# Optimization experiments

Measured on AMD Instinct MI355X. Metric: run time of the kernel, lower is better.

The kernel has to match this reference:

```python
import jax, jax.numpy as jnp
import numpy as np
from jax import lax

B, T, I, H = 64, 512, 1024, 1024


def setup_inputs() -> dict:
    key = jax.random.key(0)
    ks = jax.random.split(key, 10)
    stdv = 1.0 / np.sqrt(H)
    u = lambda k, shp: jax.random.uniform(k, shp, jnp.float32, -stdv, stdv)
    return {
        "x": jax.random.normal(ks[0], (B, T, I), jnp.float32),
        "hx": jax.random.normal(ks[1], (B, H), jnp.float32),
        "cx": jax.random.normal(ks[2], (B, H), jnp.float32),
        "weight_ih": u(ks[3], (4 * H, I)),
        "weight_hh": u(ks[4], (4 * H, H)),
        "bias_ih": u(ks[5], (4 * H,)),
        "bias_hh": u(ks[6], (4 * H,)),
        "weight_ch_i": u(ks[7], (H,)),
        "weight_ch_f": u(ks[8], (H,)),
        "weight_ch_o": u(ks[9], (H,)),
    }


def reference(x, hx, cx, weight_ih, weight_hh, bias_ih, bias_hh,
              weight_ch_i, weight_ch_f, weight_ch_o):
    # Peephole LSTM over time. Note: original module returns the INITIAL
    # (hx, cx) as the state output (faithful to source).
    bias = bias_ih + bias_hh  # fuse the two bias adds

    def step(carry, x_t):
        h, c = carry  # [B,H] each
        xh = x_t @ weight_ih.T + h @ weight_hh.T + bias  # [B,4H]
        i, f, g, o = jnp.split(xh, 4, axis=1)
        i = jax.nn.sigmoid(i + weight_ch_i * c)
        f = jax.nn.sigmoid(f + weight_ch_f * c)
        g = jnp.tanh(g)
        cy = f * c + i * g
        o = jax.nn.sigmoid(o + weight_ch_o * cy)
        hy = o * jnp.tanh(cy)
        return (hy, cy), hy

    xs = jnp.swapaxes(x, 0, 1)  # [T,B,I]
    _, hs = lax.scan(step, (hx, cx), xs)  # hs: [T,B,H]
    hidden_seq = jnp.swapaxes(hs, 0, 1)  # [B,T,H]
    return hidden_seq, (hx, cx)
```

## Files before the change

### kernel.cpp

```cpp
#include <hip/hip_runtime.h>
#include <hip/hip_bf16.h>
#include <cstdint>
#include <cstddef>

#define BB 64
#define TT 512
#define II 1024
#define HH 1024
#define NSLOT 256

typedef __attribute__((ext_vector_type(8))) short bf16x8;
typedef __attribute__((ext_vector_type(4))) float f32x4;
typedef __attribute__((ext_vector_type(8))) ushort ushort8v;
typedef __attribute__((ext_vector_type(2))) unsigned long long u64x2;

#define OFF_WHH   0ull
#define OFF_WIH   8388608ull
#define OFF_BIAS  16777216ull
#define OFF_CNT   16793600ull
#define OFF_HROT  16801792ull
#define OFF_HBUF  83910656ull
#define OFF_CBUF  84172800ull
#define OFF_PRE   84434944ull
#define OFF_XB_B  84434944ull
#define NEED_A    352870400ull
#define NEED_B    151543808ull

__device__ __forceinline__ ushort f2b(float f) {
  union { float f; uint32_t u; } v; v.f = f;
  uint32_t r = v.u + 0x7fffu + ((v.u >> 16) & 1u);
  return (ushort)(r >> 16);
}
__device__ __forceinline__ float b2f(ushort u) {
  union { uint32_t u; float f; } v; v.u = ((uint32_t)u) << 16; return v.f;
}
__device__ __forceinline__ float sigm(float x) { return 1.0f / (1.0f + __expf(-x)); }
__device__ __forceinline__ float tanh_f(float x) {
  float e = __expf(2.0f * x);
  return 1.0f - 2.0f / (e + 1.0f);
}

__global__ void k_prep(const float* __restrict__ wih, const float* __restrict__ whh,
                       const float* __restrict__ bih, const float* __restrict__ bhh,
                       const float* __restrict__ hx, const float* __restrict__ cx,
                       ushort* __restrict__ Whh_b, ushort* __restrict__ Wih_b,
                       float* __restrict__ bias, ushort* __restrict__ hbuf0,
                       float* __restrict__ cbuf, uint32_t* __restrict__ hrot,
                       int* __restrict__ cnt) {
  const int tid = blockIdx.x * blockDim.x + threadIdx.x;
  const int nth = gridDim.x * blockDim.x;
  for (int idx = tid; idx < 4096 * 128; idx += nth) {
    const size_t o = (size_t)idx * 8;
    f32x4 h0 = *(const f32x4*)(whh + o), h1 = *(const f32x4*)(whh + o + 4);
    f32x4 i0 = *(const f32x4*)(wih + o), i1 = *(const f32x4*)(wih + o + 4);
    ushort8v a, b;
    a[0]=f2b(h0[0]); a[1]=f2b(h0[1]); a[2]=f2b(h0[2]); a[3]=f2b(h0[3]);
    a[4]=f2b(h1[0]); a[5]=f2b(h1[1]); a[6]=f2b(h1[2]); a[7]=f2b(h1[3]);
    b[0]=f2b(i0[0]); b[1]=f2b(i0[1]); b[2]=f2b(i0[2]); b[3]=f2b(i0[3]);
    b[4]=f2b(i1[0]); b[5]=f2b(i1[1]); b[6]=f2b(i1[2]); b[7]=f2b(i1[3]);
    *(ushort8v*)(Whh_b + o) = a;
    *(ushort8v*)(Wih_b + o) = b;
  }
  for (int idx = tid; idx < 4096; idx += nth) bias[idx] = bih[idx] + bhh[idx];
  for (int idx = tid; idx < BB * HH; idx += nth) {
    const ushort hb = f2b(hx[idx]);
    hbuf0[idx] = hb;
    cbuf[idx] = cx[idx];
    hrot[idx] = (uint32_t)hb;
  }
  for (int idx = tid; idx < 512 * 4; idx += nth) cnt[idx] = 0;
}

__global__ void k_convx_tb(const float* __restrict__ x, ushort* __restrict__ xb) {
  const int tid = blockIdx.x * blockDim.x + threadIdx.x;
  const int nth = gridDim.x * blockDim.x;
  for (int idx = tid; idx < TT * BB * (II / 8); idx += nth) {
    const int i8 = idx & 127;
    const int tb = idx >> 7;
    const int t = tb >> 6, b = tb & 63;
    const float* src = x + ((size_t)b * TT + t) * II + (size_t)i8 * 8;
    f32x4 v0 = *(const f32x4*)src, v1 = *(const f32x4*)(src + 4);
    ushort8v o;
    o[0]=f2b(v0[0]); o[1]=f2b(v0[1]); o[2]=f2b(v0[2]); o[3]=f2b(v0[3]);
    o[4]=f2b(v1[0]); o[5]=f2b(v1[1]); o[6]=f2b(v1[2]); o[7]=f2b(v1[3]);
    *(ushort8v*)(xb + (size_t)idx * 8) = o;
  }
}

template<bool FASTA>
__global__ void __launch_bounds__(256)
k_gemm(const ushort* __restrict__ xb, const float* __restrict__ xf,
       const ushort* __restrict__ Wih, ushort* __restrict__ pre) {
  __shared__ ushort As[2][8192];
  __shared__ ushort Bs[2][8192];
  const int tid = threadIdx.x;
  const int lane = tid & 63;
  const int w = tid >> 6;
  const int wm = w & 1, wn = w >> 1;
  const int l15 = lane & 15, kg = lane >> 4;
  const int work = (blockIdx.x & 7) * 1024 + (blockIdx.x >> 3);
  const int rp = work >> 5, cp = work & 31;
  const int m0 = rp * 128, n0 = cp * 128;

  f32x4 acc[4][4];
#pragma unroll
  for (int i = 0; i < 4; ++i)
#pragma unroll
    for (int j = 0; j < 4; ++j) acc[i][j] = f32x4{0.f, 0.f, 0.f, 0.f};

  bf16x8 ra[4], rb[4];

#define LOADTILE(KT)                                                          \
  {                                                                           \
    _Pragma("unroll")                                                         \
    for (int it = 0; it < 4; ++it) {                                          \
      const int idx = it * 256 + tid;                                         \
      const int row = idx >> 3, seg = idx & 7;                                \
      if (FASTA) {                                                            \
        ra[it] = *(const bf16x8*)(xb + (size_t)(m0 + row) * 1024 + (KT) * 64 + seg * 8); \
      } else {                                                                \
        const float* s = xf + (size_t)(m0 + row) * 1024 + (KT) * 64 + seg * 8;\
        f32x4 v0 = *(const f32x4*)s, v1 = *(const f32x4*)(s + 4);             \
        bf16x8 o;                                                             \
        o[0]=(short)f2b(v0[0]); o[1]=(short)f2b(v0[1]);                       \
        o[2]=(short)f2b(v0[2]); o[3]=(short)f2b(v0[3]);                       \
        o[4]=(short)f2b(v1[0]); o[5]=(short)f2b(v1[1]);                       \
        o[6]=(short)f2b(v1[2]); o[7]=(short)f2b(v1[3]);                       \
        ra[it] = o;                                                           \
      }                                                                       \
      rb[it] = *(const bf16x8*)(Wih + (size_t)(n0 + row) * 1024 + (KT) * 64 + seg * 8); \
    }                                                                         \
  }

#define WRITETILE(BUF)                                                        \
  {                                                                           \
    _Pragma("unroll")                                                         \
    for (int it = 0; it < 4; ++it) {                                          \
      const int idx = it * 256 + tid;                                         \
      const int row = idx >> 3, seg = idx & 7;                                \
      const int off = row * 64 + ((seg ^ (row & 7)) << 3);                    \
      *(bf16x8*)(&As[BUF][off]) = ra[it];                                     \
      *(bf16x8*)(&Bs[BUF][off]) = rb[it];                                     \
    }                                                                         \
  }

  LOADTILE(0);
  WRITETILE(0);
  __syncthreads();

#pragma unroll 1
  for (int kt = 0; kt < 16; ++kt) {
    const int cur = kt & 1;
    if (kt < 15) LOADTILE(kt + 1);
#pragma unroll
    for (int ks = 0; ks < 2; ++ks) {
      bf16x8 af[4], bf_[4];
      const int koff = ks * 32 + kg * 8;
      const int swz = koff ^ ((l15 & 7) << 3);
#pragma unroll
      for (int i = 0; i < 4; ++i) {
        const int arow = wm * 64 + i * 16 + l15;
        af[i] = *(const bf16x8*)(&As[cur][arow * 64 + swz]);
        const int brow = wn * 64 + i * 16 + l15;
        bf_[i] = *(const bf16x8*)(&Bs[cur][brow * 64 + swz]);
      }
#pragma unroll
      for (int i = 0; i < 4; ++i)
#pragma unroll
        for (int j = 0; j < 4; ++j)
          acc[i][j] = __builtin_amdgcn_mfma_f32_16x16x32_bf16(af[i], bf_[j], acc[i][j], 0, 0, 0);
    }
    if (kt < 15) WRITETILE(cur ^ 1);
    __syncthreads();
  }

#pragma unroll
  for (int i = 0; i < 4; ++i)
#pragma unroll
    for (int j = 0; j < 4; ++j)
#pragma unroll
      for (int e = 0; e < 4; ++e) {
        const int m = m0 + wm * 64 + i * 16 + kg * 4 + e;
        const int n = n0 + wn * 64 + j * 16 + l15;
        pre[((size_t)(m & 511) * 64 + (m >> 9)) * 4096 + n] = f2b(acc[i][j][e]);
      }
#undef LOADTILE
#undef WRITETILE
}

__global__ void __launch_bounds__(256, 1)
k_recur(const ushort* __restrict__ Whh_b, const float* __restrict__ bias,
        uint32_t* __restrict__ hrot, const ushort* __restrict__ pre,
        const float* __restrict__ cx,
        const float* __restrict__ wci, const float* __restrict__ wcf,
        const float* __restrict__ wco, float* __restrict__ out,
        int* __restrict__ cnt) {
  __shared__ float red[4][4][16][17];
  const int tid = threadIdx.x;
  const int lane = tid & 63;
  const int w = tid >> 6;
  const int l15 = lane & 15, kg = lane >> 4;
  const int g = blockIdx.x & 3, j = blockIdx.x >> 2;

  bf16x8 wf[4][8];
#pragma unroll
  for (int gate = 0; gate < 4; ++gate)
#pragma unroll
    for (int ks = 0; ks < 8; ++ks)
      wf[gate][ks] = *(const bf16x8*)(Whh_b
          + (size_t)(gate * 1024 + j * 16 + l15) * 1024 + (w * 8 + ks) * 32 + kg * 8);

  const int grow = tid >> 4, ghl = tid & 15;
  const int brow = g * 16 + grow;
  const int hidx = j * 16 + ghl;
  const float bi = bias[hidx], bff = bias[1024 + hidx],
              bg = bias[2048 + hidx], bo = bias[3072 + hidx];
  const float pci = wci[hidx], pcf = wcf[hidx], pco = wco[hidx];
  float creg = cx[brow * 1024 + hidx];

  const int rowoff = (g * 16 + l15) * 1024 + w * 256 + kg * 8;

  const ushort* pp0 = pre + ((size_t)brow) * 4096 + hidx;
  float pxi = b2f(pp0[0]), pxf = b2f(pp0[1024]),
        pxg = b2f(pp0[2048]), pxo = b2f(pp0[3072]);

#pragma unroll 1
  for (int t = 0; t < 512; ++t) {
    const int tn = (t < 511) ? (t + 1) : 511;
    const ushort* pp = pre + ((size_t)tn * 64 + brow) * 4096 + hidx;
    const ushort ru0 = pp[0], ru1 = pp[1024], ru2 = pp[2048], ru3 = pp[3072];

    if (t > 0) {
      const int* cp = &cnt[t * 4 + g];
      while (__hip_atomic_load(cp, __ATOMIC_RELAXED, __HIP_MEMORY_SCOPE_AGENT) < 64)
        __builtin_amdgcn_s_sleep(1);
    }

    const unsigned long long* hq =
        (const unsigned long long*)(hrot + (size_t)(t & (NSLOT - 1)) * 65536 + rowoff);
    const unsigned long long pat =
        ((unsigned long long)(uint32_t)t << 48) | ((unsigned long long)(uint32_t)t << 16);
    const unsigned long long MSK = 0xFFFF0000FFFF0000ULL;
    unsigned long long q[32];
#pragma unroll
    for (int ks = 0; ks < 8; ++ks) {
      u64x2 v0 = *(const u64x2*)(hq + ks * 16);
      u64x2 v1 = *(const u64x2*)(hq + ks * 16 + 2);
      q[ks * 4 + 0] = v0[0]; q[ks * 4 + 1] = v0[1];
      q[ks * 4 + 2] = v1[0]; q[ks * 4 + 3] = v1[1];
    }
    unsigned long long bad = 0;
#pragma unroll
    for (int qq = 0; qq < 32; ++qq) bad |= (q[qq] ^ pat) & MSK;
    while (bad) {
#pragma unroll
      for (int qq = 0; qq < 32; ++qq)
        if ((q[qq] ^ pat) & MSK)
          q[qq] = __hip_atomic_load(hq + (qq >> 2) * 16 + (qq & 3),
                                    __ATOMIC_RELAXED, __HIP_MEMORY_SCOPE_AGENT);
      bad = 0;
#pragma unroll
      for (int qq = 0; qq < 32; ++qq) bad |= (q[qq] ^ pat) & MSK;
    }
    bf16x8 af[8];
#pragma unroll
    for (int ks = 0; ks < 8; ++ks) {
      const unsigned long long v0 = q[ks * 4 + 0], v1 = q[ks * 4 + 1],
                               v2 = q[ks * 4 + 2], v3 = q[ks * 4 + 3];
      bf16x8 a;
      a[0] = (short)(v0 & 0xFFFF); a[1] = (short)((v0 >> 32) & 0xFFFF);
      a[2] = (short)(v1 & 0xFFFF); a[3] = (short)((v1 >> 32) & 0xFFFF);
      a[4] = (short)(v2 & 0xFFFF); a[5] = (short)((v2 >> 32) & 0xFFFF);
      a[6] = (short)(v3 & 0xFFFF); a[7] = (short)((v3 >> 32) & 0xFFFF);
      af[ks] = a;
    }

    f32x4 acc[4];
#pragma unroll
    for (int gate = 0; gate < 4; ++gate) acc[gate] = f32x4{0.f, 0.f, 0.f, 0.f};
#pragma unroll
    for (int ks = 0; ks < 8; ++ks)
#pragma unroll
      for (int gate = 0; gate < 4; ++gate)
        acc[gate] = __builtin_amdgcn_mfma_f32_16x16x32_bf16(af[ks], wf[gate][ks], acc[gate], 0, 0, 0);

#pragma unroll
    for (int gate = 0; gate < 4; ++gate)
#pragma unroll
      for (int e = 0; e < 4; ++e)
        red[w][gate][kg * 4 + e][l15] = acc[gate][e];
    __syncthreads();

    float s0 = 0.f, s1 = 0.f, s2 = 0.f, s3 = 0.f;
#pragma unroll
    for (int ww = 0; ww < 4; ++ww) {
      s0 += red[ww][0][grow][ghl];
      s1 += red[ww][1][grow][ghl];
      s2 += red[ww][2][grow][ghl];
      s3 += red[ww][3][grow][ghl];
    }
    const float ig = sigm(s0 + bi + pxi + pci * creg);
    const float fg = sigm(s1 + bff + pxf + pcf * creg);
    const float gg = tanh_f(s2 + bg + pxg);
    const float cy = fg * creg + ig * gg;
    const float og = sigm(s3 + bo + pxo + pco * cy);
    const float hy = og * tanh_f(cy);
    creg = cy;
    if (t < 511) {
      const uint32_t word = (((uint32_t)(t + 1)) << 16) | (uint32_t)f2b(hy);
      __hip_atomic_store(&hrot[(size_t)((t + 1) & (NSLOT - 1)) * 65536 + brow * 1024 + hidx],
                         word, __ATOMIC_RELAXED, __HIP_MEMORY_SCOPE_AGENT);
      if (tid == 0)
        __hip_atomic_fetch_add(&cnt[(t + 1) * 4 + g], 1, __ATOMIC_RELAXED,
                               __HIP_MEMORY_SCOPE_AGENT);
    }
    __builtin_nontemporal_store(hy, &out[(size_t)brow * 524288 + (size_t)t * 1024 + hidx]);
    pxi = b2f(ru0); pxf = b2f(ru1); pxg = b2f(ru2); pxo = b2f(ru3);
    __syncthreads();
  }
}

template<bool XB>
__global__ void __launch_bounds__(256)
k_step2(const ushort* __restrict__ Whh, const ushort* __restrict__ Wih,
        const float* __restrict__ bias,
        const ushort* __restrict__ hprev, ushort* __restrict__ hnext,
        float* __restrict__ cbuf, const ushort* __restrict__ xb,
        const float* __restrict__ x,
        const float* __restrict__ wci, const float* __restrict__ wcf,
        const float* __restrict__ wco, float* __restrict__ out, int t) {
  __shared__ float pre[32][33];
  const int lane = threadIdx.x & 63;
  const int w = threadIdx.x >> 6;
  const int mt = w & 1, ct = w >> 1;
  const int mg = blockIdx.x & 1, cg = blockIdx.x >> 1;
  const int l15 = lane & 15, kg = lane >> 4;
  const int arow = mg * 32 + mt * 16 + l15;
  const int gate = ct * 2 + (l15 >> 3);
  const int hl = l15 & 7;
  const int gcol = gate * HH + cg * 8 + hl;

  const ushort* wr = Whh + (size_t)gcol * 1024 + kg * 8;
  const ushort* hr = hprev + (size_t)arow * HH + kg * 8;

  f32x4 acc0 = {0.f,0.f,0.f,0.f};
  f32x4 acc1 = {0.f,0.f,0.f,0.f};

#pragma unroll 8
  for (int ks = 0; ks < 32; ks += 2) {
    bf16x8 a0 = *(const bf16x8*)(hr + ks * 32);
    bf16x8 b0 = *(const bf16x8*)(wr + ks * 32);
    acc0 = __builtin_amdgcn_mfma_f32_16x16x32_bf16(a0, b0, acc0, 0, 0, 0);
    bf16x8 a1 = *(const bf16x8*)(hr + ks * 32 + 32);
    bf16x8 b1 = *(const bf16x8*)(wr + ks * 32 + 32);
    acc1 = __builtin_amdgcn_mfma_f32_16x16x32_bf16(a1, b1, acc1, 0, 0, 0);
  }
  const ushort* wrx = Wih + (size_t)gcol * 1024 + kg * 8;
  if (XB) {
    const ushort* xr = xb + ((size_t)t * BB + arow) * II + kg * 8;
#pragma unroll 8
    for (int ks = 0; ks < 32; ks += 2) {
      bf16x8 a0 = *(const bf16x8*)(xr + ks * 32);
      bf16x8 b0 = *(const bf16x8*)(wrx + ks * 32);
      acc0 = __builtin_amdgcn_mfma_f32_16x16x32_bf16(a0, b0, acc0, 0, 0, 0);
      bf16x8 a1 = *(const bf16x8*)(xr + ks * 32 + 32);
      bf16x8 b1 = *(const bf16x8*)(wrx + ks * 32 + 32);
      acc1 = __builtin_amdgcn_mfma_f32_16x16x32_bf16(a1, b1, acc1, 0, 0, 0);
    }
  } else {
    const float* xr = x + ((size_t)arow * TT + t) * II + kg * 8;
#pragma unroll 4
    for (int ks = 0; ks < 32; ++ks) {
      f32x4 v0 = *(const f32x4*)(xr + ks * 32);
      f32x4 v1 = *(const f32x4*)(xr + ks * 32 + 4);
      bf16x8 a;
      a[0]=(short)f2b(v0[0]); a[1]=(short)f2b(v0[1]);
      a[2]=(short)f2b(v0[2]); a[3]=(short)f2b(v0[3]);
      a[4]=(short)f2b(v1[0]); a[5]=(short)f2b(v1[1]);
      a[6]=(short)f2b(v1[2]); a[7]=(short)f2b(v1[3]);
      bf16x8 b0 = *(const bf16x8*)(wrx + ks * 32);
      acc0 = __builtin_amdgcn_mfma_f32_16x16x32_bf16(a, b0, acc0, 0, 0, 0);
    }
  }
  f32x4 acc = acc0 + acc1;

  const float bv = bias[gcol];
  const int lr0 = mt * 16 + kg * 4;
  const int lc2 = ct * 16 + l15;
#pragma unroll
  for (int jj = 0; jj < 4; ++jj) pre[lr0 + jj][lc2] = acc[jj] + bv;
  __syncthreads();

  const int tid = threadIdx.x;
  const int lr = tid >> 3;
  const int hl2 = tid & 7;
  const int b = mg * 32 + lr;
  const int hi = cg * 8 + hl2;
  const float ip = pre[lr][hl2];
  const float fp = pre[lr][8 + hl2];
  const float gp = pre[lr][16 + hl2];
  const float op = pre[lr][24 + hl2];
  const float c = cbuf[b * HH + hi];
  const float ig = sigm(ip + wci[hi] * c);
  const float fg = sigm(fp + wcf[hi] * c);
  const float gg = tanh_f(gp);
  const float cy = fg * c + ig * gg;
  const float og = sigm(op + wco[hi] * cy);
  const float hy = og * tanh_f(cy);
  cbuf[b * HH + hi] = cy;
  hnext[b * HH + hi] = f2b(hy);
  out[((size_t)b * TT + t) * HH + hi] = hy;
}

extern "C" void kernel_launch(void* const* d_in, const int* in_sizes, int n_in,
                              void* d_out, int out_size, void* d_ws, size_t ws_size,
                              hipStream_t stream) {
  const float* x   = (const float*)d_in[0];
  const float* hx  = (const float*)d_in[1];
  const float* cx  = (const float*)d_in[2];
  const float* wih = (const float*)d_in[3];
  const float* whh = (const float*)d_in[4];
  const float* bih = (const float*)d_in[5];
  const float* bhh = (const float*)d_in[6];
  const float* wci = (const float*)d_in[7];
  const float* wcf = (const float*)d_in[8];
  const float* wco = (const float*)d_in[9];
  float* out = (float*)d_out;

  char* ws = (char*)d_ws;
  ushort*   Whh_b = (ushort*)(ws + OFF_WHH);
  ushort*   Wih_b = (ushort*)(ws + OFF_WIH);
  float*    bias  = (float*)(ws + OFF_BIAS);
  int*      cnt   = (int*)(ws + OFF_CNT);
  uint32_t* hrot  = (uint32_t*)(ws + OFF_HROT);
  ushort*   hbuf  = (ushort*)(ws + OFF_HBUF);
  float*    cbuf  = (float*)(ws + OFF_CBUF);
  ushort*   pre   = (ushort*)(ws + OFF_PRE);

  k_prep<<<512, 256, 0, stream>>>(wih, whh, bih, bhh, hx, cx,
                                  Whh_b, Wih_b, bias, hbuf, cbuf, hrot, cnt);

  if (ws_size >= NEED_A) {
    k_gemm<false><<<8192, 256, 0, stream>>>(nullptr, x, Wih_b, pre);
    k_recur<<<256, 256, 0, stream>>>(Whh_b, bias, hrot, pre, cx,
                                     wci, wcf, wco, out, cnt);
  } else if (ws_size >= NEED_B) {
    ushort* xb = (ushort*)(ws + OFF_XB_B);
    k_convx_tb<<<1024, 256, 0, stream>>>(x, xb);
    for (int t = 0; t < TT; ++t) {
      const ushort* hp = hbuf + (size_t)(t & 1) * BB * HH;
      ushort* hn = hbuf + (size_t)((t + 1) & 1) * BB * HH;
      k_step2<true><<<256, 256, 0, stream>>>(Whh_b, Wih_b, bias, hp, hn, cbuf,
                                             xb, x, wci, wcf, wco, out, t);
    }
  } else {
    for (int t = 0; t < TT; ++t) {
      const ushort* hp = hbuf + (size_t)(t & 1) * BB * HH;
      ushort* hn = hbuf + (size_t)((t + 1) & 1) * BB * HH;
      k_step2<false><<<256, 256, 0, stream>>>(Whh_b, Wih_b, bias, hp, hn, cbuf,
                                              nullptr, x, wci, wcf, wco, out, t);
    }
  }

  hipMemcpyAsync(out + 33554432, hx, (size_t)BB * HH * 4,
                 hipMemcpyDeviceToDevice, stream);
  hipMemcpyAsync(out + 33554432 + 65536, cx, (size_t)BB * HH * 4,
                 hipMemcpyDeviceToDevice, stream);
}
```

Before: 2.889 ms.

## Drop counter barrier, shrink h ring to 4 slots, retile recurrence blocks

Removes the per-step atomic counter wait. Blocks now rely only on the timestamp tags embedded in each h word, with a short backoff sleep while polling. The h rotation buffer shrinks from 256 slots to 4, and prep marks the unused slots with an invalid tag. k_recur is retiled to 512 threads covering 8 batch rows by 32 hidden units, splitting K across 8 waves, which halves the h data each block polls. The risks are that a 4-slot ring allows overwrite races if blocks drift apart, and that the K-split doubles the shared-memory reduction, with half the threads idle during the gate math.

```diff
diff --git a/kernel.cpp b/kernel.cpp
--- a/kernel.cpp
+++ b/kernel.cpp
@@ -7,7 +7,7 @@
 #define TT 512
 #define II 1024
 #define HH 1024
-#define NSLOT 256
+#define NSLOT 4
 
 typedef __attribute__((ext_vector_type(8))) short bf16x8;
 typedef __attribute__((ext_vector_type(4))) float f32x4;
@@ -17,14 +17,13 @@
 #define OFF_WHH   0ull
 #define OFF_WIH   8388608ull
 #define OFF_BIAS  16777216ull
-#define OFF_CNT   16793600ull
-#define OFF_HROT  16801792ull
-#define OFF_HBUF  83910656ull
-#define OFF_CBUF  84172800ull
-#define OFF_PRE   84434944ull
-#define OFF_XB_B  84434944ull
-#define NEED_A    352870400ull
-#define NEED_B    151543808ull
+#define OFF_HROT  16793600ull
+#define OFF_HBUF  17842176ull
+#define OFF_CBUF  18104320ull
+#define OFF_PRE   18366464ull
+#define OFF_XB_B  18366464ull
+#define NEED_A    286801920ull
+#define NEED_B    85475328ull
 
 __device__ __forceinline__ ushort f2b(float f) {
   union { float f; uint32_t u; } v; v.f = f;
@@ -45,8 +44,7 @@
                        const float* __restrict__ hx, const float* __restrict__ cx,
                        ushort* __restrict__ Whh_b, ushort* __restrict__ Wih_b,
                        float* __restrict__ bias, ushort* __restrict__ hbuf0,
-                       float* __restrict__ cbuf, uint32_t* __restrict__ hrot,
-                       int* __restrict__ cnt) {
+                       float* __restrict__ cbuf, uint32_t* __restrict__ hrot) {
   const int tid = blockIdx.x * blockDim.x + threadIdx.x;
   const int nth = gridDim.x * blockDim.x;
   for (int idx = tid; idx < 4096 * 128; idx += nth) {
@@ -68,7 +66,8 @@
     cbuf[idx] = cx[idx];
     hrot[idx] = (uint32_t)hb;
   }
-  for (int idx = tid; idx < 512 * 4; idx += nth) cnt[idx] = 0;
+  for (int idx = tid; idx < 3 * 65536; idx += nth)
+    hrot[65536 + idx] = 0xFFFF0000u;
 }
 
 __global__ void k_convx_tb(const float* __restrict__ x, ushort* __restrict__ xb) {
@@ -188,134 +187,147 @@
 #undef WRITETILE
 }
 
-__global__ void __launch_bounds__(256, 1)
+__global__ void __launch_bounds__(512, 2)
 k_recur(const ushort* __restrict__ Whh_b, const float* __restrict__ bias,
         uint32_t* __restrict__ hrot, const ushort* __restrict__ pre,
         const float* __restrict__ cx,
         const float* __restrict__ wci, const float* __restrict__ wcf,
-        const float* __restrict__ wco, float* __restrict__ out,
-        int* __restrict__ cnt) {
-  __shared__ float red[4][4][16][17];
+        const float* __restrict__ wco, float* __restrict__ out) {
+  __shared__ float red[8][4][32][9];
   const int tid = threadIdx.x;
   const int lane = tid & 63;
   const int w = tid >> 6;
   const int l15 = lane & 15, kg = lane >> 4;
-  const int g = blockIdx.x & 3, j = blockIdx.x >> 2;
-
-  bf16x8 wf[4][8];
-#pragma unroll
-  for (int gate = 0; gate < 4; ++gate)
-#pragma unroll
-    for (int ks = 0; ks < 8; ++ks)
-      wf[gate][ks] = *(const bf16x8*)(Whh_b
-          + (size_t)(gate * 1024 + j * 16 + l15) * 1024 + (w * 8 + ks) * 32 + kg * 8);
-
-  const int grow = tid >> 4, ghl = tid & 15;
-  const int brow = g * 16 + grow;
-  const int hidx = j * 16 + ghl;
-  const float bi = bias[hidx], bff = bias[1024 + hidx],
-              bg = bias[2048 + hidx], bo = bias[3072 + hidx];
-  const float pci = wci[hidx], pcf = wcf[hidx], pco = wco[hidx];
-  float creg = cx[brow * 1024 + hidx];
-
-  const int rowoff = (g * 16 + l15) * 1024 + w * 256 + kg * 8;
-
-  const ushort* pp0 = pre + ((size_t)brow) * 4096 + hidx;
-  float pxi = b2f(pp0[0]), pxf = b2f(pp0[1024]),
-        pxg = b2f(pp0[2048]), pxo = b2f(pp0[3072]);
+  const int g = blockIdx.x & 7;
+  const int j = blockIdx.x >> 3;
+
+  bf16x8 wf[4][2][4];
+#pragma unroll
+  for (int gt = 0; gt < 4; ++gt)
+#pragma unroll
+    for (int ct = 0; ct < 2; ++ct)
+#pragma unroll
+      for (int ks = 0; ks < 4; ++ks)
+        wf[gt][ct][ks] = *(const bf16x8*)(Whh_b
+            + (size_t)(gt * 1024 + j * 32 + ct * 16 + l15) * 1024
+            + w * 128 + ks * 32 + kg * 8);
+
+  const int grow = tid & 7;
+  const int ghl = (tid >> 3) & 31;
+  const int brow = g * 8 + grow;
+  const int hidx = j * 32 + ghl;
+  float bi = 0, bff = 0, bg = 0, bo = 0, pci = 0, pcf = 0, pco = 0, creg = 0;
+  float pxi = 0, pxf = 0, pxg = 0, pxo = 0;
+  if (tid < 256) {
+    bi = bias[hidx]; bff = bias[1024 + hidx];
+    bg = bias[2048 + hidx]; bo = bias[3072 + hidx];
+    pci = wci[hidx]; pcf = wcf[hidx]; pco = wco[hidx];
+    creg = cx[brow * 1024 + hidx];
+    const ushort* pp0 = pre + ((size_t)brow) * 4096 + hidx;
+    pxi = b2f(pp0[0]); pxf = b2f(pp0[1024]);
+    pxg = b2f(pp0[2048]); pxo = b2f(pp0[3072]);
+  }
+
+  const int arow = g * 8 + (l15 & 7);
+  const unsigned long long MSK = 0xFFFF0000FFFF0000ULL;
 
 #pragma unroll 1
   for (int t = 0; t < 512; ++t) {
-    const int tn = (t < 511) ? (t + 1) : 511;
-    const ushort* pp = pre + ((size_t)tn * 64 + brow) * 4096 + hidx;
-    const ushort ru0 = pp[0], ru1 = pp[1024], ru2 = pp[2048], ru3 = pp[3072];
-
-    if (t > 0) {
-      const int* cp = &cnt[t * 4 + g];
-      while (__hip_atomic_load(cp, __ATOMIC_RELAXED, __HIP_MEMORY_SCOPE_AGENT) < 64)
-        __builtin_amdgcn_s_sleep(1);
-    }
-
-    const unsigned long long* hq =
-        (const unsigned long long*)(hrot + (size_t)(t & (NSLOT - 1)) * 65536 + rowoff);
+    ushort nx0 = 0, nx1 = 0, nx2 = 0, nx3 = 0;
+    if (tid < 256) {
+      const int tn = (t < 511) ? (t + 1) : 511;
+      const ushort* pp = pre + ((size_t)tn * 64 + brow) * 4096 + hidx;
+      nx0 = pp[0]; nx1 = pp[1024]; nx2 = pp[2048]; nx3 = pp[3072];
+    }
+
+    const unsigned long long* hq = (const unsigned long long*)
+        (hrot + (size_t)(t & (NSLOT - 1)) * 65536 + (size_t)arow * 1024
+         + w * 128 + kg * 8);
     const unsigned long long pat =
         ((unsigned long long)(uint32_t)t << 48) | ((unsigned long long)(uint32_t)t << 16);
-    const unsigned long long MSK = 0xFFFF0000FFFF0000ULL;
-    unsigned long long q[32];
-#pragma unroll
-    for (int ks = 0; ks < 8; ++ks) {
-      u64x2 v0 = *(const u64x2*)(hq + ks * 16);
-      u64x2 v1 = *(const u64x2*)(hq + ks * 16 + 2);
-      q[ks * 4 + 0] = v0[0]; q[ks * 4 + 1] = v0[1];
-      q[ks * 4 + 2] = v1[0]; q[ks * 4 + 3] = v1[1];
+    unsigned long long q[16];
+#pragma unroll
+    for (int ks = 0; ks < 4; ++ks) {
+      u64x2 a = *(const u64x2*)(hq + ks * 16);
+      u64x2 b = *(const u64x2*)(hq + ks * 16 + 2);
+      q[ks * 4 + 0] = a[0]; q[ks * 4 + 1] = a[1];
+      q[ks * 4 + 2] = b[0]; q[ks * 4 + 3] = b[1];
     }
     unsigned long long bad = 0;
 #pragma unroll
-    for (int qq = 0; qq < 32; ++qq) bad |= (q[qq] ^ pat) & MSK;
+    for (int qq = 0; qq < 16; ++qq) bad |= (q[qq] ^ pat) & MSK;
+    int spins = 0;
     while (bad) {
-#pragma unroll
-      for (int qq = 0; qq < 32; ++qq)
+      if (spins++ > 2) __builtin_amdgcn_s_sleep(1);
+#pragma unroll
+      for (int qq = 0; qq < 16; ++qq)
         if ((q[qq] ^ pat) & MSK)
           q[qq] = __hip_atomic_load(hq + (qq >> 2) * 16 + (qq & 3),
                                     __ATOMIC_RELAXED, __HIP_MEMORY_SCOPE_AGENT);
       bad = 0;
 #pragma unroll
-      for (int qq = 0; qq < 32; ++qq) bad |= (q[qq] ^ pat) & MSK;
-    }
-    bf16x8 af[8];
-#pragma unroll
-    for (int ks = 0; ks < 8; ++ks) {
+      for (int qq = 0; qq < 16; ++qq) bad |= (q[qq] ^ pat) & MSK;
+    }
+
+    f32x4 acc[4][2];
+#pragma unroll
+    for (int gt = 0; gt < 4; ++gt)
+#pragma unroll
+      for (int ct = 0; ct < 2; ++ct) acc[gt][ct] = f32x4{0.f, 0.f, 0.f, 0.f};
+#pragma unroll
+    for (int ks = 0; ks < 4; ++ks) {
       const unsigned long long v0 = q[ks * 4 + 0], v1 = q[ks * 4 + 1],
                                v2 = q[ks * 4 + 2], v3 = q[ks * 4 + 3];
-      bf16x8 a;
-      a[0] = (short)(v0 & 0xFFFF); a[1] = (short)((v0 >> 32) & 0xFFFF);
-      a[2] = (short)(v1 & 0xFFFF); a[3] = (short)((v1 >> 32) & 0xFFFF);
-      a[4] = (short)(v2 & 0xFFFF); a[5] = (short)((v2 >> 32) & 0xFFFF);
-      a[6] = (short)(v3 & 0xFFFF); a[7] = (short)((v3 >> 32) & 0xFFFF);
-      af[ks] = a;
-    }
-
-    f32x4 acc[4];
-#pragma unroll
-    for (int gate = 0; gate < 4; ++gate) acc[gate] = f32x4{0.f, 0.f, 0.f, 0.f};
-#pragma unroll
-    for (int ks = 0; ks < 8; ++ks)
-#pragma unroll
-      for (int gate = 0; gate < 4; ++gate)
-        acc[gate] = __builtin_amdgcn_mfma_f32_16x16x32_bf16(af[ks], wf[gate][ks], acc[gate], 0, 0, 0);
-
-#pragma unroll
-    for (int gate = 0; gate < 4; ++gate)
-#pragma unroll
-      for (int e = 0; e < 4; ++e)
-        red[w][gate][kg * 4 + e][l15] = acc[gate][e];
+      bf16x8 af;
+      af[0] = (short)(v0 & 0xFFFF); af[1] = (short)((v0 >> 32) & 0xFFFF);
+      af[2] = (short)(v1 & 0xFFFF); af[3] = (short)((v1 >> 32) & 0xFFFF);
+      af[4] = (short)(v2 & 0xFFFF); af[5] = (short)((v2 >> 32) & 0xFFFF);
+      af[6] = (short)(v3 & 0xFFFF); af[7] = (short)((v3 >> 32) & 0xFFFF);
+#pragma unroll
+      for (int gt = 0; gt < 4; ++gt)
+#pragma unroll
+        for (int ct = 0; ct < 2; ++ct)
+          acc[gt][ct] = __builtin_amdgcn_mfma_f32_16x16x32_bf16(
+              af, wf[gt][ct][ks], acc[gt][ct], 0, 0, 0);
+    }
+
+    if (kg < 2) {
+#pragma unroll
+      for (int gt = 0; gt < 4; ++gt)
+#pragma unroll
+        for (int ct = 0; ct < 2; ++ct)
+#pragma unroll
+          for (int e = 0; e < 4; ++e)
+            red[w][gt][ct * 16 + l15][kg * 4 + e] = acc[gt][ct][e];
+    }
     __syncthreads();
 
-    float s0 = 0.f, s1 = 0.f, s2 = 0.f, s3 = 0.f;
-#pragma unroll
-    for (int ww = 0; ww < 4; ++ww) {
-      s0 += red[ww][0][grow][ghl];
-      s1 += red[ww][1][grow][ghl];
-      s2 += red[ww][2][grow][ghl];
-      s3 += red[ww][3][grow][ghl];
-    }
-    const float ig = sigm(s0 + bi + pxi + pci * creg);
-    const float fg = sigm(s1 + bff + pxf + pcf * creg);
-    const float gg = tanh_f(s2 + bg + pxg);
-    const float cy = fg * creg + ig * gg;
-    const float og = sigm(s3 + bo + pxo + pco * cy);
-    const float hy = og * tanh_f(cy);
-    creg = cy;
-    if (t < 511) {
-      const uint32_t word = (((uint32_t)(t + 1)) << 16) | (uint32_t)f2b(hy);
-      __hip_atomic_store(&hrot[(size_t)((t + 1) & (NSLOT - 1)) * 65536 + brow * 1024 + hidx],
-                         word, __ATOMIC_RELAXED, __HIP_MEMORY_SCOPE_AGENT);
-      if (tid == 0)
-        __hip_atomic_fetch_add(&cnt[(t + 1) * 4 + g], 1, __ATOMIC_RELAXED,
-                               __HIP_MEMORY_SCOPE_AGENT);
-    }
-    __builtin_nontemporal_store(hy, &out[(size_t)brow * 524288 + (size_t)t * 1024 + hidx]);
-    pxi = b2f(ru0); pxf = b2f(ru1); pxg = b2f(ru2); pxo = b2f(ru3);
+    if (tid < 256) {
+      float s0 = 0.f, s1 = 0.f, s2 = 0.f, s3 = 0.f;
+#pragma unroll
+      for (int ww = 0; ww < 8; ++ww) {
+        s0 += red[ww][0][ghl][grow];
+        s1 += red[ww][1][ghl][grow];
+        s2 += red[ww][2][ghl][grow];
+        s3 += red[ww][3][ghl][grow];
+      }
+      const float ig = sigm(s0 + bi + pxi + pci * creg);
+      const float fg = sigm(s1 + bff + pxf + pcf * creg);
+      const float gg = tanh_f(s2 + bg + pxg);
+      const float cy = fg * creg + ig * gg;
+      const float og = sigm(s3 + bo + pxo + pco * cy);
+      const float hy = og * tanh_f(cy);
+      creg = cy;
+      if (t < 511) {
+        const uint32_t word = (((uint32_t)(t + 1)) << 16) | (uint32_t)f2b(hy);
+        __hip_atomic_store(&hrot[(size_t)((t + 1) & (NSLOT - 1)) * 65536
+                                 + brow * 1024 + hidx],
+                           word, __ATOMIC_RELAXED, __HIP_MEMORY_SCOPE_AGENT);
+      }
+      __builtin_nontemporal_store(hy,
+          &out[(size_t)brow * 524288 + (size_t)t * 1024 + hidx]);
+      pxi = b2f(nx0); pxf = b2f(nx1); pxg = b2f(nx2); pxo = b2f(nx3);
+    }
     __syncthreads();
   }
 }
@@ -431,19 +443,18 @@
   ushort*   Whh_b = (ushort*)(ws + OFF_WHH);
   ushort*   Wih_b = (ushort*)(ws + OFF_WIH);
   float*    bias  = (float*)(ws + OFF_BIAS);
-  int*      cnt   = (int*)(ws + OFF_CNT);
   uint32_t* hrot  = (uint32_t*)(ws + OFF_HROT);
   ushort*   hbuf  = (ushort*)(ws + OFF_HBUF);
   float*    cbuf  = (float*)(ws + OFF_CBUF);
   ushort*   pre   = (ushort*)(ws + OFF_PRE);
 
   k_prep<<<512, 256, 0, stream>>>(wih, whh, bih, bhh, hx, cx,
-                                  Whh_b, Wih_b, bias, hbuf, cbuf, hrot, cnt);
+                                  Whh_b, Wih_b, bias, hbuf, cbuf, hrot);
 
   if (ws_size >= NEED_A) {
     k_gemm<false><<<8192, 256, 0, stream>>>(nullptr, x, Wih_b, pre);
-    k_recur<<<256, 256, 0, stream>>>(Whh_b, bias, hrot, pre, cx,
-                                     wci, wcf, wco, out, cnt);
+    k_recur<<<256, 512, 0, stream>>>(Whh_b, bias, hrot, pre, cx,
+                                     wci, wcf, wco, out);
   } else if (ws_size >= NEED_B) {
     ushort* xb = (ushort*)(ws + OFF_XB_B);
     k_convx_tb<<<1024, 256, 0, stream>>>(x, xb);
```

After: 3.572 ms. +23.6%, slower.

## Restructure persistent LSTM recurrence into 128 blocks cycling over four batch groups

Applied to the files above, without the earlier changes.

The persistent recurrence kernel now uses 128 blocks, each owning 8 hidden units across all four gates and looping over the four 16-row batch groups in turn. The counter-based barrier is gone: readiness is detected only through per-element timestamp tags, with hrot slots pre-filled with invalid tags. The next group's hidden-state loads are prefetched optimistically before the current MFMA, and the LDS reduction buffer is double-buffered so one __syncthreads per group replaces two per step. The aim is to hide inter-block synchronisation latency by pipelining groups, at the cost of half as many blocks, only half the threads doing the pointwise gate math, and a larger prep-kernel initialisation.

```diff
diff --git a/kernel.cpp b/kernel.cpp
--- a/kernel.cpp
+++ b/kernel.cpp
@@ -7,24 +7,23 @@
 #define TT 512
 #define II 1024
 #define HH 1024
-#define NSLOT 256
+#define CSLOT 256
 
 typedef __attribute__((ext_vector_type(8))) short bf16x8;
 typedef __attribute__((ext_vector_type(4))) float f32x4;
 typedef __attribute__((ext_vector_type(8))) ushort ushort8v;
-typedef __attribute__((ext_vector_type(2))) unsigned long long u64x2;
+typedef __attribute__((ext_vector_type(4))) unsigned int u32x4;
 
 #define OFF_WHH   0ull
 #define OFF_WIH   8388608ull
 #define OFF_BIAS  16777216ull
-#define OFF_CNT   16793600ull
-#define OFF_HROT  16801792ull
-#define OFF_HBUF  83910656ull
-#define OFF_CBUF  84172800ull
-#define OFF_PRE   84434944ull
-#define OFF_XB_B  84434944ull
-#define NEED_A    352870400ull
-#define NEED_B    151543808ull
+#define OFF_HROT  16793600ull
+#define OFF_HBUF  83902464ull
+#define OFF_CBUF  84164608ull
+#define OFF_PRE   84426752ull
+#define OFF_XB_B  84426752ull
+#define NEED_A    352862208ull
+#define NEED_B    151535616ull
 
 __device__ __forceinline__ ushort f2b(float f) {
   union { float f; uint32_t u; } v; v.f = f;
@@ -45,8 +44,7 @@
                        const float* __restrict__ hx, const float* __restrict__ cx,
                        ushort* __restrict__ Whh_b, ushort* __restrict__ Wih_b,
                        float* __restrict__ bias, ushort* __restrict__ hbuf0,
-                       float* __restrict__ cbuf, uint32_t* __restrict__ hrot,
-                       int* __restrict__ cnt) {
+                       float* __restrict__ cbuf, uint32_t* __restrict__ hrot) {
   const int tid = blockIdx.x * blockDim.x + threadIdx.x;
   const int nth = gridDim.x * blockDim.x;
   for (int idx = tid; idx < 4096 * 128; idx += nth) {
@@ -62,13 +60,18 @@
     *(ushort8v*)(Wih_b + o) = b;
   }
   for (int idx = tid; idx < 4096; idx += nth) bias[idx] = bih[idx] + bhh[idx];
+  for (int idx = tid; idx < 4 * CSLOT * 16384; idx += nth) {
+    const int slot = (idx >> 14) & (CSLOT - 1);
+    if (slot != 0) hrot[idx] = 0xFFFF0000u;
+  }
   for (int idx = tid; idx < BB * HH; idx += nth) {
     const ushort hb = f2b(hx[idx]);
     hbuf0[idx] = hb;
     cbuf[idx] = cx[idx];
-    hrot[idx] = (uint32_t)hb;
-  }
-  for (int idx = tid; idx < 512 * 4; idx += nth) cnt[idx] = 0;
+    const int brow = idx >> 10, hh = idx & 1023;
+    const int g = brow >> 4, r = brow & 15;
+    hrot[(size_t)g * CSLOT * 16384 + r * 1024 + hh] = (uint32_t)hb;
+  }
 }
 
 __global__ void k_convx_tb(const float* __restrict__ x, ushort* __restrict__ xb) {
@@ -193,130 +196,160 @@
         uint32_t* __restrict__ hrot, const ushort* __restrict__ pre,
         const float* __restrict__ cx,
         const float* __restrict__ wci, const float* __restrict__ wcf,
-        const float* __restrict__ wco, float* __restrict__ out,
-        int* __restrict__ cnt) {
-  __shared__ float red[4][4][16][17];
+        const float* __restrict__ wco, float* __restrict__ out) {
+  __shared__ float red[2][4][2][16][17];
   const int tid = threadIdx.x;
   const int lane = tid & 63;
   const int w = tid >> 6;
   const int l15 = lane & 15, kg = lane >> 4;
-  const int g = blockIdx.x & 3, j = blockIdx.x >> 2;
-
-  bf16x8 wf[4][8];
-#pragma unroll
-  for (int gate = 0; gate < 4; ++gate)
+  const int jb = blockIdx.x;
+
+  bf16x8 wf[2][8];
+#pragma unroll
+  for (int nt = 0; nt < 2; ++nt) {
+    const int c = nt * 16 + l15;
+    const size_t gcol = (size_t)((c >> 3) * 1024 + jb * 8 + (c & 7));
 #pragma unroll
     for (int ks = 0; ks < 8; ++ks)
-      wf[gate][ks] = *(const bf16x8*)(Whh_b
-          + (size_t)(gate * 1024 + j * 16 + l15) * 1024 + (w * 8 + ks) * 32 + kg * 8);
-
-  const int grow = tid >> 4, ghl = tid & 15;
-  const int brow = g * 16 + grow;
-  const int hidx = j * 16 + ghl;
-  const float bi = bias[hidx], bff = bias[1024 + hidx],
-              bg = bias[2048 + hidx], bo = bias[3072 + hidx];
-  const float pci = wci[hidx], pcf = wcf[hidx], pco = wco[hidx];
-  float creg = cx[brow * 1024 + hidx];
-
-  const int rowoff = (g * 16 + l15) * 1024 + w * 256 + kg * 8;
-
-  const ushort* pp0 = pre + ((size_t)brow) * 4096 + hidx;
-  float pxi = b2f(pp0[0]), pxf = b2f(pp0[1024]),
-        pxg = b2f(pp0[2048]), pxo = b2f(pp0[3072]);
+      wf[nt][ks] = *(const bf16x8*)(Whh_b + gcol * 1024 + w * 256 + ks * 32 + kg * 8);
+  }
+
+  const int grow = (tid >> 3) & 15;
+  const int hoff = tid & 7;
+  const int hidx = jb * 8 + hoff;
+  float bi = 0, bff = 0, bg = 0, bo = 0, pci = 0, pcf = 0, pco = 0;
+  float c0 = 0, c1 = 0, c2 = 0, c3 = 0;
+  if (tid < 128) {
+    bi = bias[hidx]; bff = bias[1024 + hidx];
+    bg = bias[2048 + hidx]; bo = bias[3072 + hidx];
+    pci = wci[hidx]; pcf = wcf[hidx]; pco = wco[hidx];
+    c0 = cx[(0 * 16 + grow) * 1024 + hidx];
+    c1 = cx[(1 * 16 + grow) * 1024 + hidx];
+    c2 = cx[(2 * 16 + grow) * 1024 + hidx];
+    c3 = cx[(3 * 16 + grow) * 1024 + hidx];
+  }
+
+  const int lrow = l15;
+  const int loff = w * 256 + kg * 8;
+  uint32_t q[64];
+  ushort nxp0 = 0, nxp1 = 0, nxp2 = 0, nxp3 = 0;
+
+  {
+    const uint32_t* hw = hrot + (size_t)lrow * 1024 + loff;
+#pragma unroll
+    for (int ks = 0; ks < 8; ++ks) {
+      u32x4 a = *(const u32x4*)(hw + ks * 32);
+      u32x4 b = *(const u32x4*)(hw + ks * 32 + 4);
+      q[ks*8+0]=a[0]; q[ks*8+1]=a[1]; q[ks*8+2]=a[2]; q[ks*8+3]=a[3];
+      q[ks*8+4]=b[0]; q[ks*8+5]=b[1]; q[ks*8+6]=b[2]; q[ks*8+7]=b[3];
+    }
+    if (tid < 128) {
+      const ushort* pq = pre + (size_t)grow * 4096 + hidx;
+      nxp0 = pq[0]; nxp1 = pq[1024]; nxp2 = pq[2048]; nxp3 = pq[3072];
+    }
+  }
 
 #pragma unroll 1
   for (int t = 0; t < 512; ++t) {
-    const int tn = (t < 511) ? (t + 1) : 511;
-    const ushort* pp = pre + ((size_t)tn * 64 + brow) * 4096 + hidx;
-    const ushort ru0 = pp[0], ru1 = pp[1024], ru2 = pp[2048], ru3 = pp[3072];
-
-    if (t > 0) {
-      const int* cp = &cnt[t * 4 + g];
-      while (__hip_atomic_load(cp, __ATOMIC_RELAXED, __HIP_MEMORY_SCOPE_AGENT) < 64)
-        __builtin_amdgcn_s_sleep(1);
-    }
-
-    const unsigned long long* hq =
-        (const unsigned long long*)(hrot + (size_t)(t & (NSLOT - 1)) * 65536 + rowoff);
-    const unsigned long long pat =
-        ((unsigned long long)(uint32_t)t << 48) | ((unsigned long long)(uint32_t)t << 16);
-    const unsigned long long MSK = 0xFFFF0000FFFF0000ULL;
-    unsigned long long q[32];
-#pragma unroll
-    for (int ks = 0; ks < 8; ++ks) {
-      u64x2 v0 = *(const u64x2*)(hq + ks * 16);
-      u64x2 v1 = *(const u64x2*)(hq + ks * 16 + 2);
-      q[ks * 4 + 0] = v0[0]; q[ks * 4 + 1] = v0[1];
-      q[ks * 4 + 2] = v1[0]; q[ks * 4 + 3] = v1[1];
-    }
-    unsigned long long bad = 0;
-#pragma unroll
-    for (int qq = 0; qq < 32; ++qq) bad |= (q[qq] ^ pat) & MSK;
-    while (bad) {
-#pragma unroll
-      for (int qq = 0; qq < 32; ++qq)
-        if ((q[qq] ^ pat) & MSK)
-          q[qq] = __hip_atomic_load(hq + (qq >> 2) * 16 + (qq & 3),
-                                    __ATOMIC_RELAXED, __HIP_MEMORY_SCOPE_AGENT);
-      bad = 0;
-#pragma unroll
-      for (int qq = 0; qq < 32; ++qq) bad |= (q[qq] ^ pat) & MSK;
-    }
-    bf16x8 af[8];
-#pragma unroll
-    for (int ks = 0; ks < 8; ++ks) {
-      const unsigned long long v0 = q[ks * 4 + 0], v1 = q[ks * 4 + 1],
-                               v2 = q[ks * 4 + 2], v3 = q[ks * 4 + 3];
-      bf16x8 a;
-      a[0] = (short)(v0 & 0xFFFF); a[1] = (short)((v0 >> 32) & 0xFFFF);
-      a[2] = (short)(v1 & 0xFFFF); a[3] = (short)((v1 >> 32) & 0xFFFF);
-      a[4] = (short)(v2 & 0xFFFF); a[5] = (short)((v2 >> 32) & 0xFFFF);
-      a[6] = (short)(v3 & 0xFFFF); a[7] = (short)((v3 >> 32) & 0xFFFF);
-      af[ks] = a;
-    }
-
-    f32x4 acc[4];
-#pragma unroll
-    for (int gate = 0; gate < 4; ++gate) acc[gate] = f32x4{0.f, 0.f, 0.f, 0.f};
-#pragma unroll
-    for (int ks = 0; ks < 8; ++ks)
-#pragma unroll
-      for (int gate = 0; gate < 4; ++gate)
-        acc[gate] = __builtin_amdgcn_mfma_f32_16x16x32_bf16(af[ks], wf[gate][ks], acc[gate], 0, 0, 0);
-
-#pragma unroll
-    for (int gate = 0; gate < 4; ++gate)
-#pragma unroll
-      for (int e = 0; e < 4; ++e)
-        red[w][gate][kg * 4 + e][l15] = acc[gate][e];
-    __syncthreads();
-
-    float s0 = 0.f, s1 = 0.f, s2 = 0.f, s3 = 0.f;
-#pragma unroll
-    for (int ww = 0; ww < 4; ++ww) {
-      s0 += red[ww][0][grow][ghl];
-      s1 += red[ww][1][grow][ghl];
-      s2 += red[ww][2][grow][ghl];
-      s3 += red[ww][3][grow][ghl];
-    }
-    const float ig = sigm(s0 + bi + pxi + pci * creg);
-    const float fg = sigm(s1 + bff + pxf + pcf * creg);
-    const float gg = tanh_f(s2 + bg + pxg);
-    const float cy = fg * creg + ig * gg;
-    const float og = sigm(s3 + bo + pxo + pco * cy);
-    const float hy = og * tanh_f(cy);
-    creg = cy;
-    if (t < 511) {
-      const uint32_t word = (((uint32_t)(t + 1)) << 16) | (uint32_t)f2b(hy);
-      __hip_atomic_store(&hrot[(size_t)((t + 1) & (NSLOT - 1)) * 65536 + brow * 1024 + hidx],
-                         word, __ATOMIC_RELAXED, __HIP_MEMORY_SCOPE_AGENT);
-      if (tid == 0)
-        __hip_atomic_fetch_add(&cnt[(t + 1) * 4 + g], 1, __ATOMIC_RELAXED,
-                               __HIP_MEMORY_SCOPE_AGENT);
-    }
-    __builtin_nontemporal_store(hy, &out[(size_t)brow * 524288 + (size_t)t * 1024 + hidx]);
-    pxi = b2f(ru0); pxf = b2f(ru1); pxg = b2f(ru2); pxo = b2f(ru3);
-    __syncthreads();
+#pragma unroll
+    for (int g = 0; g < 4; ++g) {
+      const int pb = g & 1;
+      const uint32_t tg = (uint32_t)t << 16;
+      uint32_t bad = 0;
+#pragma unroll
+      for (int i = 0; i < 64; ++i) bad |= (q[i] ^ tg);
+      if (bad >> 16) {
+        const uint32_t* hq = hrot
+            + ((size_t)(g * CSLOT + (t & (CSLOT - 1)))) * 16384
+            + (size_t)lrow * 1024 + loff;
+        for (;;) {
+#pragma unroll
+          for (int i = 0; i < 64; ++i)
+            if ((q[i] ^ tg) >> 16)
+              q[i] = __hip_atomic_load(hq + (i >> 3) * 32 + (i & 7),
+                                       __ATOMIC_RELAXED, __HIP_MEMORY_SCOPE_AGENT);
+          bad = 0;
+#pragma unroll
+          for (int i = 0; i < 64; ++i) bad |= (q[i] ^ tg);
+          if (!(bad >> 16)) break;
+          __builtin_amdgcn_s_sleep(1);
+        }
+      }
+      bf16x8 af[8];
+#pragma unroll
+      for (int ks = 0; ks < 8; ++ks) {
+        bf16x8 a;
+        a[0]=(short)(q[ks*8+0]&0xFFFF); a[1]=(short)(q[ks*8+1]&0xFFFF);
+        a[2]=(short)(q[ks*8+2]&0xFFFF); a[3]=(short)(q[ks*8+3]&0xFFFF);
+        a[4]=(short)(q[ks*8+4]&0xFFFF); a[5]=(short)(q[ks*8+5]&0xFFFF);
+        a[6]=(short)(q[ks*8+6]&0xFFFF); a[7]=(short)(q[ks*8+7]&0xFFFF);
+        af[ks] = a;
+      }
+      {
+        const int g2 = (g + 1) & 3;
+        const int t2 = t + (g == 3);
+        const uint32_t* hw = hrot
+            + ((size_t)(g2 * CSLOT + (t2 & (CSLOT - 1)))) * 16384
+            + (size_t)lrow * 1024 + loff;
+#pragma unroll
+        for (int ks = 0; ks < 8; ++ks) {
+          u32x4 a = *(const u32x4*)(hw + ks * 32);
+          u32x4 b = *(const u32x4*)(hw + ks * 32 + 4);
+          q[ks*8+0]=a[0]; q[ks*8+1]=a[1]; q[ks*8+2]=a[2]; q[ks*8+3]=a[3];
+          q[ks*8+4]=b[0]; q[ks*8+5]=b[1]; q[ks*8+6]=b[2]; q[ks*8+7]=b[3];
+        }
+      }
+      f32x4 acc0 = {0.f,0.f,0.f,0.f}, acc1 = acc0;
+#pragma unroll
+      for (int ks = 0; ks < 8; ++ks) {
+        acc0 = __builtin_amdgcn_mfma_f32_16x16x32_bf16(af[ks], wf[0][ks], acc0, 0, 0, 0);
+        acc1 = __builtin_amdgcn_mfma_f32_16x16x32_bf16(af[ks], wf[1][ks], acc1, 0, 0, 0);
+      }
+#pragma unroll
+      for (int e = 0; e < 4; ++e) {
+        red[pb][w][0][kg * 4 + e][l15] = acc0[e];
+        red[pb][w][1][kg * 4 + e][l15] = acc1[e];
+      }
+      float pxi = 0, pxf = 0, pxg = 0, pxo = 0;
+      ushort nn0 = 0, nn1 = 0, nn2 = 0, nn3 = 0;
+      if (tid < 128) {
+        pxi = b2f(nxp0); pxf = b2f(nxp1); pxg = b2f(nxp2); pxo = b2f(nxp3);
+        const int g2 = (g + 1) & 3;
+        const int t2p = (g == 3) ? ((t < 511) ? t + 1 : 511) : t;
+        const ushort* pq = pre + ((size_t)t2p * 64 + g2 * 16 + grow) * 4096 + hidx;
+        nn0 = pq[0]; nn1 = pq[1024]; nn2 = pq[2048]; nn3 = pq[3072];
+      }
+      __syncthreads();
+      if (tid < 128) {
+        float s0 = 0, s1 = 0, s2 = 0, s3 = 0;
+#pragma unroll
+        for (int ww = 0; ww < 4; ++ww) {
+          s0 += red[pb][ww][0][grow][hoff];
+          s1 += red[pb][ww][0][grow][8 + hoff];
+          s2 += red[pb][ww][1][grow][hoff];
+          s3 += red[pb][ww][1][grow][8 + hoff];
+        }
+        float creg = (g == 0) ? c0 : (g == 1) ? c1 : (g == 2) ? c2 : c3;
+        const float ig = sigm(s0 + bi + pxi + pci * creg);
+        const float fg = sigm(s1 + bff + pxf + pcf * creg);
+        const float gg = tanh_f(s2 + bg + pxg);
+        const float cy = fg * creg + ig * gg;
+        const float og = sigm(s3 + bo + pxo + pco * cy);
+        const float hy = og * tanh_f(cy);
+        if (g == 0) c0 = cy; else if (g == 1) c1 = cy;
+        else if (g == 2) c2 = cy; else c3 = cy;
+        if (t < 511) {
+          const uint32_t word = (((uint32_t)(t + 1)) << 16) | (uint32_t)f2b(hy);
+          __hip_atomic_store(
+              &hrot[((size_t)(g * CSLOT + ((t + 1) & (CSLOT - 1)))) * 16384
+                    + (size_t)grow * 1024 + hidx],
+              word, __ATOMIC_RELAXED, __HIP_MEMORY_SCOPE_AGENT);
+        }
+        __builtin_nontemporal_store(hy,
+            &out[(size_t)(g * 16 + grow) * 524288 + (size_t)t * 1024 + hidx]);
+        nxp0 = nn0; nxp1 = nn1; nxp2 = nn2; nxp3 = nn3;
+      }
+    }
   }
 }
 
@@ -431,19 +464,18 @@
   ushort*   Whh_b = (ushort*)(ws + OFF_WHH);
   ushort*   Wih_b = (ushort*)(ws + OFF_WIH);
   float*    bias  = (float*)(ws + OFF_BIAS);
-  int*      cnt   = (int*)(ws + OFF_CNT);
   uint32_t* hrot  = (uint32_t*)(ws + OFF_HROT);
   ushort*   hbuf  = (ushort*)(ws + OFF_HBUF);
   float*    cbuf  = (float*)(ws + OFF_CBUF);
   ushort*   pre   = (ushort*)(ws + OFF_PRE);
 
   k_prep<<<512, 256, 0, stream>>>(wih, whh, bih, bhh, hx, cx,
-                                  Whh_b, Wih_b, bias, hbuf, cbuf, hrot, cnt);
+                                  Whh_b, Wih_b, bias, hbuf, cbuf, hrot);
 
   if (ws_size >= NEED_A) {
     k_gemm<false><<<8192, 256, 0, stream>>>(nullptr, x, Wih_b, pre);
-    k_recur<<<256, 256, 0, stream>>>(Whh_b, bias, hrot, pre, cx,
-                                     wci, wcf, wco, out, cnt);
+    k_recur<<<128, 256, 0, stream>>>(Whh_b, bias, hrot, pre, cx,
+                                     wci, wcf, wco, out);
   } else if (ws_size >= NEED_B) {
     ushort* xb = (ushort*)(ws + OFF_XB_B);
     k_convx_tb<<<1024, 256, 0, stream>>>(x, xb);
```

After: 5.037 ms. 74.4% more time.

## Restructure recurrent hidden-state ring per batch group with single-thread counter polling

Applied to the files above, without the earlier changes.

Reorganizes the rotating hidden-state buffer so each of the four batch groups owns a contiguous slot region, and pre-fills non-initial slots with an invalid tag. Counter polling moves to one thread followed by a block barrier, replacing per-thread spinning. Per-element tag checks now read 32-bit words with a sleep in the retry loop. The next-step preactivation prefetch moves after the hidden-state load, and the trailing barrier is dropped. The aim is to cut atomic polling traffic and memory contention in the step-to-step handoff, at the cost of an extra barrier per step and a larger init pass.

```diff
diff --git a/kernel.cpp b/kernel.cpp
--- a/kernel.cpp
+++ b/kernel.cpp
@@ -7,12 +7,12 @@
 #define TT 512
 #define II 1024
 #define HH 1024
-#define NSLOT 256
+#define CSLOT 256
 
 typedef __attribute__((ext_vector_type(8))) short bf16x8;
 typedef __attribute__((ext_vector_type(4))) float f32x4;
 typedef __attribute__((ext_vector_type(8))) ushort ushort8v;
-typedef __attribute__((ext_vector_type(2))) unsigned long long u64x2;
+typedef __attribute__((ext_vector_type(4))) unsigned int u32x4;
 
 #define OFF_WHH   0ull
 #define OFF_WIH   8388608ull
@@ -62,11 +62,17 @@
     *(ushort8v*)(Wih_b + o) = b;
   }
   for (int idx = tid; idx < 4096; idx += nth) bias[idx] = bih[idx] + bhh[idx];
+  for (int idx = tid; idx < 4 * CSLOT * 16384; idx += nth) {
+    const int slot = (idx >> 14) & (CSLOT - 1);
+    if (slot != 0) hrot[idx] = 0xFFFF0000u;
+  }
   for (int idx = tid; idx < BB * HH; idx += nth) {
     const ushort hb = f2b(hx[idx]);
     hbuf0[idx] = hb;
     cbuf[idx] = cx[idx];
-    hrot[idx] = (uint32_t)hb;
+    const int brow = idx >> 10, hh = idx & 1023;
+    const int g = brow >> 4, r = brow & 15;
+    hrot[(size_t)g * CSLOT * 16384 + (size_t)r * 1024 + hh] = (uint32_t)hb;
   }
   for (int idx = tid; idx < 512 * 4; idx += nth) cnt[idx] = 0;
 }
@@ -218,7 +224,8 @@
   const float pci = wci[hidx], pcf = wcf[hidx], pco = wco[hidx];
   float creg = cx[brow * 1024 + hidx];
 
-  const int rowoff = (g * 16 + l15) * 1024 + w * 256 + kg * 8;
+  const size_t gbase = (size_t)g * CSLOT * 16384;
+  const int rowoff = l15 * 1024 + w * 256 + kg * 8;
 
   const ushort* pp0 = pre + ((size_t)brow) * 4096 + hidx;
   float pxi = b2f(pp0[0]), pxf = b2f(pp0[1024]),
@@ -226,54 +233,53 @@
 
 #pragma unroll 1
   for (int t = 0; t < 512; ++t) {
+    if (t > 0) {
+      if (tid == 0) {
+        const int* cp = &cnt[t * 4 + g];
+        while (__hip_atomic_load(cp, __ATOMIC_RELAXED, __HIP_MEMORY_SCOPE_AGENT) < 64)
+          __builtin_amdgcn_s_sleep(1);
+      }
+      __syncthreads();
+    }
+
+    const uint32_t* hp = hrot + gbase + (size_t)(t & (CSLOT - 1)) * 16384 + rowoff;
+    const uint32_t tg = (uint32_t)t << 16;
+    uint32_t q[64];
+#pragma unroll
+    for (int ks = 0; ks < 8; ++ks) {
+      u32x4 a = *(const u32x4*)(hp + ks * 32);
+      u32x4 b = *(const u32x4*)(hp + ks * 32 + 4);
+      q[ks*8+0]=a[0]; q[ks*8+1]=a[1]; q[ks*8+2]=a[2]; q[ks*8+3]=a[3];
+      q[ks*8+4]=b[0]; q[ks*8+5]=b[1]; q[ks*8+6]=b[2]; q[ks*8+7]=b[3];
+    }
+    uint32_t bad = 0;
+#pragma unroll
+    for (int i = 0; i < 64; ++i) bad |= (q[i] ^ tg);
+    while (bad >> 16) {
+#pragma unroll
+      for (int i = 0; i < 64; ++i)
+        if ((q[i] ^ tg) >> 16)
+          q[i] = __hip_atomic_load(hp + (i >> 3) * 32 + (i & 7),
+                                   __ATOMIC_RELAXED, __HIP_MEMORY_SCOPE_AGENT);
+      bad = 0;
+#pragma unroll
+      for (int i = 0; i < 64; ++i) bad |= (q[i] ^ tg);
+      if (bad >> 16) __builtin_amdgcn_s_sleep(1);
+    }
+    bf16x8 af[8];
+#pragma unroll
+    for (int ks = 0; ks < 8; ++ks) {
+      bf16x8 a;
+      a[0]=(short)(q[ks*8+0]&0xFFFF); a[1]=(short)(q[ks*8+1]&0xFFFF);
+      a[2]=(short)(q[ks*8+2]&0xFFFF); a[3]=(short)(q[ks*8+3]&0xFFFF);
+      a[4]=(short)(q[ks*8+4]&0xFFFF); a[5]=(short)(q[ks*8+5]&0xFFFF);
+      a[6]=(short)(q[ks*8+6]&0xFFFF); a[7]=(short)(q[ks*8+7]&0xFFFF);
+      af[ks] = a;
+    }
+
     const int tn = (t < 511) ? (t + 1) : 511;
     const ushort* pp = pre + ((size_t)tn * 64 + brow) * 4096 + hidx;
-    const ushort ru0 = pp[0], ru1 = pp[1024], ru2 = pp[2048], ru3 = pp[3072];
-
-    if (t > 0) {
-      const int* cp = &cnt[t * 4 + g];
-      while (__hip_atomic_load(cp, __ATOMIC_RELAXED, __HIP_MEMORY_SCOPE_AGENT) < 64)
-        __builtin_amdgcn_s_sleep(1);
-    }
-
-    const unsigned long long* hq =
-        (const unsigned long long*)(hrot + (size_t)(t & (NSLOT - 1)) * 65536 + rowoff);
-    const unsigned long long pat =
-        ((unsigned long long)(uint32_t)t << 48) | ((unsigned long long)(uint32_t)t << 16);
-    const unsigned long long MSK = 0xFFFF0000FFFF0000ULL;
-    unsigned long long q[32];
-#pragma unroll
-    for (int ks = 0; ks < 8; ++ks) {
-      u64x2 v0 = *(const u64x2*)(hq + ks * 16);
-      u64x2 v1 = *(const u64x2*)(hq + ks * 16 + 2);
-      q[ks * 4 + 0] = v0[0]; q[ks * 4 + 1] = v0[1];
-      q[ks * 4 + 2] = v1[0]; q[ks * 4 + 3] = v1[1];
-    }
-    unsigned long long bad = 0;
-#pragma unroll
-    for (int qq = 0; qq < 32; ++qq) bad |= (q[qq] ^ pat) & MSK;
-    while (bad) {
-#pragma unroll
-      for (int qq = 0; qq < 32; ++qq)
-        if ((q[qq] ^ pat) & MSK)
-          q[qq] = __hip_atomic_load(hq + (qq >> 2) * 16 + (qq & 3),
-                                    __ATOMIC_RELAXED, __HIP_MEMORY_SCOPE_AGENT);
-      bad = 0;
-#pragma unroll
-      for (int qq = 0; qq < 32; ++qq) bad |= (q[qq] ^ pat) & MSK;
-    }
-    bf16x8 af[8];
-#pragma unroll
-    for (int ks = 0; ks < 8; ++ks) {
-      const unsigned long long v0 = q[ks * 4 + 0], v1 = q[ks * 4 + 1],
-                               v2 = q[ks * 4 + 2], v3 = q[ks * 4 + 3];
-      bf16x8 a;
-      a[0] = (short)(v0 & 0xFFFF); a[1] = (short)((v0 >> 32) & 0xFFFF);
-      a[2] = (short)(v1 & 0xFFFF); a[3] = (short)((v1 >> 32) & 0xFFFF);
-      a[4] = (short)(v2 & 0xFFFF); a[5] = (short)((v2 >> 32) & 0xFFFF);
-      a[6] = (short)(v3 & 0xFFFF); a[7] = (short)((v3 >> 32) & 0xFFFF);
-      af[ks] = a;
-    }
+    const ushort nn0 = pp[0], nn1 = pp[1024], nn2 = pp[2048], nn3 = pp[3072];
 
     f32x4 acc[4];
 #pragma unroll
@@ -308,15 +314,16 @@
     creg = cy;
     if (t < 511) {
       const uint32_t word = (((uint32_t)(t + 1)) << 16) | (uint32_t)f2b(hy);
-      __hip_atomic_store(&hrot[(size_t)((t + 1) & (NSLOT - 1)) * 65536 + brow * 1024 + hidx],
+      __hip_atomic_store(&hrot[gbase + (size_t)((t + 1) & (CSLOT - 1)) * 16384
+                               + (size_t)grow * 1024 + hidx],
                          word, __ATOMIC_RELAXED, __HIP_MEMORY_SCOPE_AGENT);
       if (tid == 0)
         __hip_atomic_fetch_add(&cnt[(t + 1) * 4 + g], 1, __ATOMIC_RELAXED,
                                __HIP_MEMORY_SCOPE_AGENT);
     }
-    __builtin_nontemporal_store(hy, &out[(size_t)brow * 524288 + (size_t)t * 1024 + hidx]);
-    pxi = b2f(ru0); pxf = b2f(ru1); pxg = b2f(ru2); pxo = b2f(ru3);
-    __syncthreads();
+    __builtin_nontemporal_store(hy,
+        &out[(size_t)brow * 524288 + (size_t)t * 1024 + hidx]);
+    pxi = b2f(nn0); pxf = b2f(nn1); pxg = b2f(nn2); pxo = b2f(nn3);
   }
 }
 
```

Result: slower. 2.958 ms (+2.4%).
